# Kernel optimization log

Measured on AMD Instinct MI355X. Metric: run time of the kernel, lower is better.

## Reference

```python
import jax, jax.numpy as jnp
import numpy as np


def setup_inputs() -> dict:
    key = jax.random.key(0)
    H, W, N = 4096, 4096, 8
    label = jax.random.randint(key, (H, W), 0, N, dtype=jnp.int64 if jax.config.read('jax_enable_x64') else jnp.int32).astype(jnp.int32)
    return {"label": label, "N": N}


def reference(label, N):
    # torch: eye(N).index_select(0, label.view(-1)).view(H, W, N).permute(2, 0, 1)
    # == one_hot over last axis, then move class axis to front -> (N, H, W)
    oh = jax.nn.one_hot(label, N, dtype=jnp.float32)  # (H, W, N)
    return jnp.transpose(oh, (2, 0, 1))  # (N, H, W)
```

## Files before the change

kernel.cpp:

```cpp
#include <hip/hip_runtime.h>
#include <hip/hip_bf16.h>

__global__ void __launch_bounds__(256) get_one_hot_59442347376951_kernel(
    const int* __restrict__ label, float* __restrict__ out,
    int total , int N) {
    long long i = ((long long)blockIdx.x * blockDim.x + threadIdx.x) * 4;
    if (i >= total) return;

    int4 lab = *reinterpret_cast<const int4*>(label + i);

    for (int n = 0; n < N; ++n) {
        float4 v;
        v.x = (lab.x == n) ? 1.0f : 0.0f;
        v.y = (lab.y == n) ? 1.0f : 0.0f;
        v.z = (lab.z == n) ? 1.0f : 0.0f;
        v.w = (lab.w == n) ? 1.0f : 0.0f;
        *reinterpret_cast<float4*>(out + (long long)n * total + i) = v;
    }
}

extern "C" void kernel_launch(void* const* d_in, const int* in_sizes, int n_in,
                              void* d_out, int out_size, void* d_ws, size_t ws_size,
                              hipStream_t stream) {
    const int* label = (const int*)d_in[0];
    float* out = (float*)d_out;

    int total = in_sizes[0];
    int N = out_size / total;

    int threads = total / 4;
    int block = 256;
    int grid = (threads + block - 1) / block;

    get_one_hot_59442347376951_kernel<<<grid, block, 0, stream>>>(label, out, total, N);
}
```

Baseline: 130.4 us.

## Assign one class plane per wavefront with staggered chunk iteration for N=8

Adds a specialized kernel for N=8, used when the size divides evenly. Each 512-thread block covers a 4096-element chunk, and each of its 8 wavefronts writes one class plane. Wavefronts start at staggered positions in the chunk so that different planes are written concurrently while label loads are shared through cache. The goal is more bytes in flight per thread and better spread of the write streams. The cost is that each wavefront reloads the labels, which relies on L1/L2 hits. A generic fallback kernel handles other shapes.

```diff
diff --git a/kernel.cpp b/kernel.cpp
--- a/kernel.cpp
+++ b/kernel.cpp
@@ -1,14 +1,40 @@
 #include <hip/hip_runtime.h>
 #include <hip/hip_bf16.h>
 
-__global__ void __launch_bounds__(256) get_one_hot_59442347376951_kernel(
+#define CHUNK 4096
+#define ITERS 16
+
+__global__ void __launch_bounds__(512) get_one_hot_59442347376951_kernel(
     const int* __restrict__ label, float* __restrict__ out,
-    int total , int N) {
+    int total ) {
+    const int w    = threadIdx.x >> 6;
+    const int lane = threadIdx.x & 63;
+
+    const long long base      = (long long)blockIdx.x * CHUNK;
+    const long long planeBase = (long long)w * total;
+
+    for (int it = 0; it < ITERS; ++it) {
+        int j = (it + 2 * w) & (ITERS - 1);
+        long long idx = base + j * 256 + lane * 4;
+
+        int4 lab = *reinterpret_cast<const int4*>(label + idx);
+
+        float4 v;
+        v.x = (lab.x == w) ? 1.0f : 0.0f;
+        v.y = (lab.y == w) ? 1.0f : 0.0f;
+        v.z = (lab.z == w) ? 1.0f : 0.0f;
+        v.w = (lab.w == w) ? 1.0f : 0.0f;
+
+        *reinterpret_cast<float4*>(out + planeBase + idx) = v;
+    }
+}
+
+__global__ void __launch_bounds__(256) get_one_hot_generic_kernel(
+    const int* __restrict__ label, float* __restrict__ out,
+    int total, int N) {
     long long i = ((long long)blockIdx.x * blockDim.x + threadIdx.x) * 4;
     if (i >= total) return;
-
     int4 lab = *reinterpret_cast<const int4*>(label + i);
-
     for (int n = 0; n < N; ++n) {
         float4 v;
         v.x = (lab.x == n) ? 1.0f : 0.0f;
@@ -28,9 +54,11 @@
     int total = in_sizes[0];
     int N = out_size / total;
 
-    int threads = total / 4;
-    int block = 256;
-    int grid = (threads + block - 1) / block;
-
-    get_one_hot_59442347376951_kernel<<<grid, block, 0, stream>>>(label, out, total, N);
+    if (N == 8 && total % CHUNK == 0) {
+        int grid = total / CHUNK;
+        get_one_hot_59442347376951_kernel<<<grid, 512, 0, stream>>>(label, out, total);
+    } else {
+        int grid = (total / 4 + 255) / 256;
+        get_one_hot_generic_kernel<<<grid, 256, 0, stream>>>(label, out, total, N);
+    }
 }
```

After: 152.9 us. 1.17x slower.

## Pack labels to bytes, then expand one class plane per grid row

Applied to the files above, without the earlier changes.

Adds a pre-pass that packs the int32 labels into bytes in the workspace. A second kernel, launched with a 2D grid, has each block write a contiguous span of a single class plane from the packed labels. This replaces the old pattern where each thread wrote to all N planes, which spread stores across widely separated addresses, and it shrinks the data re-read per plane. The cost is an extra kernel launch, an extra 16MB write and re-read of the packed buffer, and per-thread 64B-strided stores. A fallback generic path handles cases where N is above 256 or the size is not a multiple of 4096.

```diff
diff --git a/kernel.cpp b/kernel.cpp
--- a/kernel.cpp
+++ b/kernel.cpp
@@ -1,14 +1,50 @@
 #include <hip/hip_runtime.h>
 #include <hip/hip_bf16.h>
 
-__global__ void __launch_bounds__(256) get_one_hot_59442347376951_kernel(
+
+typedef unsigned int u32;
+
+__global__ void __launch_bounds__(256) pack_labels_kernel(
+    const int* __restrict__ label, u32* __restrict__ packed, int total) {
+    int t = blockIdx.x * 256 + threadIdx.x;
+    long long i = (long long)t * 16;
+    if (i >= total) return;
+    const int4* lp = reinterpret_cast<const int4*>(label + i);
+    int4 a = lp[0], b = lp[1], c = lp[2], d = lp[3];
+    u32 p0 = (u32)(a.x & 255) | ((u32)(a.y & 255) << 8) | ((u32)(a.z & 255) << 16) | ((u32)(a.w & 255) << 24);
+    u32 p1 = (u32)(b.x & 255) | ((u32)(b.y & 255) << 8) | ((u32)(b.z & 255) << 16) | ((u32)(b.w & 255) << 24);
+    u32 p2 = (u32)(c.x & 255) | ((u32)(c.y & 255) << 8) | ((u32)(c.z & 255) << 16) | ((u32)(c.w & 255) << 24);
+    u32 p3 = (u32)(d.x & 255) | ((u32)(d.y & 255) << 8) | ((u32)(d.z & 255) << 16) | ((u32)(d.w & 255) << 24);
+    reinterpret_cast<uint4*>(packed)[t] = make_uint4(p0, p1, p2, p3);
+}
+
+__global__ void __launch_bounds__(256) expand_kernel(
+    const u32* __restrict__ packed, float* __restrict__ out, int total) {
+    const u32 n = blockIdx.y;
+    int t = blockIdx.x * 256 + threadIdx.x;
+    long long i = (long long)t * 16;
+
+    uint4 p = reinterpret_cast<const uint4*>(packed)[t];
+    u32 w[4] = {p.x, p.y, p.z, p.w};
+    float4* op = reinterpret_cast<float4*>(out + (long long)n * total + i);
+
+#pragma unroll
+    for (int k = 0; k < 4; ++k) {
+        float4 v;
+        v.x = (((w[k]      ) & 255u) == n) ? 1.0f : 0.0f;
+        v.y = (((w[k] >> 8 ) & 255u) == n) ? 1.0f : 0.0f;
+        v.z = (((w[k] >> 16) & 255u) == n) ? 1.0f : 0.0f;
+        v.w = (((w[k] >> 24)       ) == n) ? 1.0f : 0.0f;
+        op[k] = v;
+    }
+}
+
+__global__ void __launch_bounds__(256) get_one_hot_generic_kernel(
     const int* __restrict__ label, float* __restrict__ out,
-    int total , int N) {
+    int total, int N) {
     long long i = ((long long)blockIdx.x * blockDim.x + threadIdx.x) * 4;
     if (i >= total) return;
-
     int4 lab = *reinterpret_cast<const int4*>(label + i);
-
     for (int n = 0; n < N; ++n) {
         float4 v;
         v.x = (lab.x == n) ? 1.0f : 0.0f;
@@ -28,9 +64,14 @@
     int total = in_sizes[0];
     int N = out_size / total;
 
-    int threads = total / 4;
-    int block = 256;
-    int grid = (threads + block - 1) / block;
-
-    get_one_hot_59442347376951_kernel<<<grid, block, 0, stream>>>(label, out, total, N);
+    bool fast = (N <= 256) && (total % 4096 == 0) && (ws_size >= (size_t)total);
+    if (fast) {
+        int blocks = total / 4096;
+        pack_labels_kernel<<<blocks, 256, 0, stream>>>(label, (u32*)d_ws, total);
+        dim3 grid(blocks, N);
+        expand_kernel<<<grid, 256, 0, stream>>>((const u32*)d_ws, out, total);
+    } else {
+        int grid = (total / 4 + 255) / 256;
+        get_one_hot_generic_kernel<<<grid, 256, 0, stream>>>(label, out, total, N);
+    }
 }
```

Result: slower. 184.6 us (+41.6%).

## Split one-hot into bit-packing pass and per-class bitmask expansion pass

Applied to the files above, without the earlier changes.

For N=8, a first kernel packs each label's three bits into per-class 32-bit bitmasks stored in the workspace. A second kernel, launched with one grid row per class, expands those bitmasks into contiguous float4 writes for a single class plane. The aim is to make each block's output stream touch only one class plane and to shrink the data read in the write-heavy pass. In exchange it adds a second launch and extra workspace traffic. It also treats labels by their low three bits, so out-of-range labels would not produce zero rows.

```diff
diff --git a/kernel.cpp b/kernel.cpp
--- a/kernel.cpp
+++ b/kernel.cpp
@@ -1,14 +1,64 @@
 #include <hip/hip_runtime.h>
 #include <hip/hip_bf16.h>
 
-__global__ void __launch_bounds__(256) get_one_hot_59442347376951_kernel(
+
+typedef unsigned int u32;
+
+__global__ void __launch_bounds__(256) pack_bits_kernel(
+    const int* __restrict__ label, u32* __restrict__ bits, int total) {
+    int words = total >> 5;
+    int t = blockIdx.x * 256 + threadIdx.x;
+    if (t >= words) return;
+    const int4* lp = reinterpret_cast<const int4*>(label) + (long long)t * 8;
+    u32 b0 = 0, b1 = 0, b2 = 0;
+#pragma unroll
+    for (int q = 0; q < 8; ++q) {
+        int4 a = lp[q];
+        int j = q * 4;
+        b0 |= (u32)(a.x & 1) << j;      b1 |= (u32)((a.x >> 1) & 1) << j;      b2 |= (u32)((a.x >> 2) & 1) << j;
+        b0 |= (u32)(a.y & 1) << (j+1);  b1 |= (u32)((a.y >> 1) & 1) << (j+1);  b2 |= (u32)((a.y >> 2) & 1) << (j+1);
+        b0 |= (u32)(a.z & 1) << (j+2);  b1 |= (u32)((a.z >> 1) & 1) << (j+2);  b2 |= (u32)((a.z >> 2) & 1) << (j+2);
+        b0 |= (u32)(a.w & 1) << (j+3);  b1 |= (u32)((a.w >> 1) & 1) << (j+3);  b2 |= (u32)((a.w >> 2) & 1) << (j+3);
+    }
+    u32 n0 = ~b0, n1 = ~b1, n2 = ~b2;
+    bits[0 * words + t] = n2 & n1 & n0;
+    bits[1 * words + t] = n2 & n1 & b0;
+    bits[2 * words + t] = n2 & b1 & n0;
+    bits[3 * words + t] = n2 & b1 & b0;
+    bits[4 * words + t] = b2 & n1 & n0;
+    bits[5 * words + t] = b2 & n1 & b0;
+    bits[6 * words + t] = b2 & b1 & n0;
+    bits[7 * words + t] = b2 & b1 & b0;
+}
+
+__global__ void __launch_bounds__(256) expand_bits_kernel(
+    const u32* __restrict__ bits, float* __restrict__ out, int total) {
+    const int n = blockIdx.y;
+    const int tid = threadIdx.x;
+    const int words = total >> 5;
+    const u32* wp = bits + (long long)n * words + (long long)blockIdx.x * 256;
+    float* op = out + (long long)n * total + (long long)blockIdx.x * 8192;
+    const int sh = (tid & 7) * 4;
+    const int wofs = tid >> 3;
+#pragma unroll
+    for (int it = 0; it < 8; ++it) {
+        u32 w = wp[it * 32 + wofs];
+        u32 nib = w >> sh;
+        float4 v;
+        v.x = (nib & 1u) ? 1.0f : 0.0f;
+        v.y = (nib & 2u) ? 1.0f : 0.0f;
+        v.z = (nib & 4u) ? 1.0f : 0.0f;
+        v.w = (nib & 8u) ? 1.0f : 0.0f;
+        *reinterpret_cast<float4*>(op + it * 1024 + tid * 4) = v;
+    }
+}
+
+__global__ void __launch_bounds__(256) get_one_hot_generic_kernel(
     const int* __restrict__ label, float* __restrict__ out,
-    int total , int N) {
+    int total, int N) {
     long long i = ((long long)blockIdx.x * blockDim.x + threadIdx.x) * 4;
     if (i >= total) return;
-
     int4 lab = *reinterpret_cast<const int4*>(label + i);
-
     for (int n = 0; n < N; ++n) {
         float4 v;
         v.x = (lab.x == n) ? 1.0f : 0.0f;
@@ -28,9 +78,14 @@
     int total = in_sizes[0];
     int N = out_size / total;
 
-    int threads = total / 4;
-    int block = 256;
-    int grid = (threads + block - 1) / block;
-
-    get_one_hot_59442347376951_kernel<<<grid, block, 0, stream>>>(label, out, total, N);
+    bool fast = (N == 8) && (total % 8192 == 0) && (ws_size >= (size_t)total);
+    if (fast) {
+        int words = total >> 5;
+        pack_bits_kernel<<<words / 256, 256, 0, stream>>>(label, (u32*)d_ws, total);
+        dim3 grid(total / 8192, N);
+        expand_bits_kernel<<<grid, 256, 0, stream>>>((const u32*)d_ws, out, total);
+    } else {
+        int grid = (total / 4 + 255) / 256;
+        get_one_hot_generic_kernel<<<grid, 256, 0, stream>>>(label, out, total, N);
+    }
 }
```

Result: no change. 128.0 us (-1.8%).
